# Kernel optimization log

Measured on AMD Instinct MI355X. Metric: run time of the kernel, lower is better.

## Reference

```python
import jax, jax.numpy as jnp
import numpy as np

COMMITMENT_COST = 0.25


def setup_inputs() -> dict:
    key = jax.random.key(0)
    k1, k2 = jax.random.split(key)
    B, H, W, D, K = 64, 32, 32, 64, 512
    inputs = jax.random.normal(k1, (B, H, W, D), dtype=jnp.float32)
    # VarianceScaling(): truncated normal with stddev ~ sqrt(1/fan_in); plain normal scaled is fine as init
    embeddings = jax.random.normal(k2, (D, K), dtype=jnp.float32) * np.float32(1.0 / np.sqrt(D))
    return {"inputs": inputs, "embeddings": embeddings}


def reference(inputs, embeddings):
    D = embeddings.shape[0]
    flat = inputs.reshape(-1, D)  # [N, D]
    distances = (
        jnp.sum(flat * flat, axis=1, keepdims=True)
        - 2.0 * (flat @ embeddings)
        + jnp.sum(embeddings * embeddings, axis=0, keepdims=True)
    )
    encoding_indices = jnp.argmin(distances, axis=1)  # [N]
    # one-hot @ embeddings.T is just a gather of rows of embeddings.T
    quantized = jnp.take(embeddings.T, encoding_indices, axis=0).reshape(inputs.shape)
    loss = (
        jnp.mean(jnp.square(jax.lax.stop_gradient(quantized) - inputs))
        + COMMITMENT_COST * jnp.mean(jnp.square(quantized - jax.lax.stop_gradient(inputs)))
    )
    # straight-through estimator
    quantized_st = inputs + jax.lax.stop_gradient(quantized - inputs)
    indices = encoding_indices.reshape(inputs.shape[:-1])
    return quantized_st, indices, loss
```

## Files before the change

### kernel.cpp

```cpp
#include <hip/hip_runtime.h>
#include <stdint.h>


#define DDIM 64
#define KCODES 512

typedef __bf16 bf16x8 __attribute__((ext_vector_type(8)));
typedef float f32x4 __attribute__((ext_vector_type(4)));

#define GLOAD_LDS16(gp, lp)                                        \
  __builtin_amdgcn_global_load_lds(                                \
      (const __attribute__((address_space(1))) void*)(gp),         \
      (__attribute__((address_space(3))) void*)(lp), 16, 0, 0)


__device__ __forceinline__ void split3(float f, __bf16& h1, __bf16& h2,
                                       __bf16& h3) {
  h1 = (__bf16)f;
  float r1 = f - (float)h1;
  h2 = (__bf16)r1;
  float r2 = r1 - (float)h2;
  h3 = (__bf16)r2;
}

__global__ void vq_prep_m(const float* __restrict__ w,
                          bf16x8* __restrict__ wb,
                          float* __restrict__ wT, float* __restrict__ wsq,
                          float* __restrict__ loss_out) {
  const int b = blockIdx.x, t = threadIdx.x;
  if (b < 16) {
    const int c = b * 256 + t;
    const int ctg = c >> 7;
    const int h = (c >> 6) & 1;
    const int L = c & 63, quad = L >> 4, col = L & 15;
    bf16x8 v1, v2, v3;
#pragma unroll
    for (int j = 0; j < 8; ++j) {
      float f = w[(quad * 8 + 32 * h + j) * KCODES + ctg * 16 + col];
      __bf16 h1, h2, h3; split3(f, h1, h2, h3);
      v1[j] = h1; v2[j] = h2; v3[j] = h3;
    }
    const int base = (ctg >> 2) * 24 + (ctg & 3) * 6 + h * 3;
    wb[(base + 0) * 64 + L] = v1;
    wb[(base + 1) * 64 + L] = v2;
    wb[(base + 2) * 64 + L] = v3;
  } else {
    int g = (b - 16) * 256 + t;
    int d = g >> 9, k = g & 511;
    wT[k * DDIM + d] = w[g];
    if (g < KCODES) {
      float s = 0.f;
      for (int dd = 0; dd < DDIM; ++dd) {
        float tv = w[dd * KCODES + g];
        s = fmaf(tv, tv, s);
      }
      wsq[g] = s;
    }
    if (g == 0) *loss_out = 0.f;
  }
}

__global__ __launch_bounds__(512, 4)
void vq_mfma(const float* __restrict__ x_in, const bf16x8* __restrict__ wb,
             const float* __restrict__ wsq, const float* __restrict__ wT,
             float* __restrict__ out_q, float* __restrict__ out_idx,
             float* __restrict__ loss_out) {
  __shared__ bf16x8 ldsb[3072];
  __shared__ unsigned long long sm_key[128];
  __shared__ float sm_xsq[128];
  __shared__ unsigned int sm_idx[128];
  __shared__ float sm_loss[128];

  const int t = threadIdx.x, b = blockIdx.x;
  const int wv = t >> 6, L = t & 63, quad = L >> 4, col = L & 15;

  const int sgbase = wv * 64 + L;

#pragma unroll
  for (int i = 0; i < 3; ++i)
    GLOAD_LDS16(wb + i * 512 + sgbase, &ldsb[i * 512 + wv * 64]);

  bf16x8 a[3][2];
  {
    const float* xr =
        x_in + ((size_t)b * 128 + wv * 16 + col) * DDIM + quad * 8;
    float ssq = 0.f;
#pragma unroll
    for (int h = 0; h < 2; ++h) {
      float4 p0 = *(const float4*)(xr + 32 * h);
      float4 p1 = *(const float4*)(xr + 32 * h + 4);
      float f[8] = {p0.x, p0.y, p0.z, p0.w, p1.x, p1.y, p1.z, p1.w};
      bf16x8 v1, v2, v3;
#pragma unroll
      for (int j = 0; j < 8; ++j) {
        ssq = fmaf(f[j], f[j], ssq);
        __bf16 h1, h2, h3; split3(f[j], h1, h2, h3);
        v1[j] = h1; v2[j] = h2; v3[j] = h3;
      }
      a[0][h] = v1; a[1][h] = v2; a[2][h] = v3;
    }
    ssq += __shfl_xor(ssq, 16, 64);
    ssq += __shfl_xor(ssq, 32, 64);
    if (quad == 0) sm_xsq[wv * 16 + col] = ssq;
  }

  float best[4];
  int bidx[4];
#pragma unroll
  for (int r = 0; r < 4; ++r) { best[r] = 3.0e38f; bidx[r] = 0; }

#pragma unroll 1
  for (int ph = 0; ph < 8; ++ph) {
    __syncthreads();
    float wq0 = wsq[ph * 64 + col];
    float wq1 = wsq[ph * 64 + 16 + col];
    float wq2 = wsq[ph * 64 + 32 + col];
    float wq3 = wsq[ph * 64 + 48 + col];
    if (ph < 7) {
      const bf16x8* src = wb + (ph + 1) * 1536 + sgbase;
      bf16x8* dst = &ldsb[((ph + 1) & 1) * 1536 + wv * 64];
#pragma unroll
      for (int i = 0; i < 3; ++i)
        GLOAD_LDS16(src + i * 512, dst + i * 512);
    }

    const bf16x8* bufp = ldsb + (ph & 1) * 1536;
    __builtin_amdgcn_s_setprio(1);
#pragma unroll
    for (int ct = 0; ct < 4; ++ct) {
      f32x4 acc = {0.f, 0.f, 0.f, 0.f};
#pragma unroll
      for (int h = 0; h < 2; ++h) {
        bf16x8 b0 = bufp[(ct * 6 + h * 3 + 0) * 64 + L];
        bf16x8 b1 = bufp[(ct * 6 + h * 3 + 1) * 64 + L];
        bf16x8 b2 = bufp[(ct * 6 + h * 3 + 2) * 64 + L];
        acc = __builtin_amdgcn_mfma_f32_16x16x32_bf16(a[0][h], b0, acc, 0, 0, 0);
        acc = __builtin_amdgcn_mfma_f32_16x16x32_bf16(a[0][h], b1, acc, 0, 0, 0);
        acc = __builtin_amdgcn_mfma_f32_16x16x32_bf16(a[1][h], b0, acc, 0, 0, 0);
        acc = __builtin_amdgcn_mfma_f32_16x16x32_bf16(a[1][h], b1, acc, 0, 0, 0);
        acc = __builtin_amdgcn_mfma_f32_16x16x32_bf16(a[0][h], b2, acc, 0, 0, 0);
        acc = __builtin_amdgcn_mfma_f32_16x16x32_bf16(a[2][h], b0, acc, 0, 0, 0);
      }
      int code = ph * 64 + ct * 16 + col;
      float wq = (ct == 0) ? wq0 : (ct == 1) ? wq1 : (ct == 2) ? wq2 : wq3;
#pragma unroll
      for (int r = 0; r < 4; ++r) {
        float d0 = fmaf(acc[r], -2.0f, wq);
        if (d0 < best[r]) { best[r] = d0; bidx[r] = code; }
      }
    }
    __builtin_amdgcn_s_setprio(0);
  }

#pragma unroll
  for (int r = 0; r < 4; ++r) {
    unsigned int ub = __float_as_uint(best[r]);
    ub = (ub & 0x80000000u) ? ~ub : (ub | 0x80000000u);
    unsigned long long key = ((unsigned long long)ub << 32) |
                             (unsigned long long)(unsigned int)bidx[r];
#pragma unroll
    for (int off = 1; off < 16; off <<= 1) {
      unsigned long long o = __shfl_xor(key, off, 64);
      key = o < key ? o : key;
    }
    if (col == 0)
      sm_key[wv * 16 + quad * 4 + r] = key;
  }
  __syncthreads();

  if (t < 128) {
    unsigned long long k = sm_key[t];
    unsigned int idx = (unsigned int)k;
    sm_idx[t] = idx;
    out_idx[(size_t)b * 128 + t] = (float)idx;
    unsigned int u = (unsigned int)(k >> 32);
    u = (u & 0x80000000u) ? (u & 0x7FFFFFFFu) : ~u;
    sm_loss[t] = (__uint_as_float(u) + sm_xsq[t]) * (1.25f / 4194304.0f);
  }
  __syncthreads();

  float4* dst = (float4*)(out_q + (size_t)b * 8192);
#pragma unroll
  for (int i = 0; i < 4; ++i) {
    int e4 = i * 512 + t;
    int p2 = e4 >> 4, d4 = e4 & 15;
    unsigned int idx = sm_idx[p2];
    dst[e4] = ((const float4*)(wT + (size_t)idx * DDIM))[d4];
  }

  if (t < 64) {
    float s = sm_loss[t] + sm_loss[t + 64];
#pragma unroll
    for (int off = 32; off > 0; off >>= 1) s += __shfl_down(s, off);
    if (t == 0) atomicAdd(loss_out, s);
  }
}


__global__ void vq_prep(const float* __restrict__ w, float* __restrict__ wT,
                        float* __restrict__ wsq, float* __restrict__ loss_out) {
  int g = blockIdx.x * 256 + threadIdx.x;
  int d = g >> 9, k = g & 511;
  wT[k * DDIM + d] = w[g];
  if (g < KCODES) {
    float s = 0.f;
    for (int dd = 0; dd < DDIM; ++dd) {
      float t = w[dd * KCODES + g];
      s = fmaf(t, t, s);
    }
    wsq[g] = s;
  }
  if (g == 0) *loss_out = 0.f;
}

__global__ __launch_bounds__(512, 8)
void vq_main(const float* __restrict__ x_in, const float* __restrict__ w,
             const float* __restrict__ wT, const float* __restrict__ wsq,
             float* __restrict__ out_q, float* __restrict__ out_idx,
             float* __restrict__ loss_out) {
  __shared__ float xs[DDIM][65];
  __shared__ unsigned long long sm_key[8][64];
  __shared__ unsigned int sm_idx[64];
  __shared__ float sm_sx[64];
  __shared__ float sm_loss[64];

  const int t = threadIdx.x;
  const int pb = blockIdx.x;
  const int wv = __builtin_amdgcn_readfirstlane(t >> 6);
  const int lane = t & 63;

  {
    const float4* src = (const float4*)(x_in + (size_t)pb * 4096);
#pragma unroll
    for (int i = 0; i < 2; ++i) {
      int e4 = i * 512 + t;
      float4 v = src[e4];
      int e = e4 << 2;
      int pt = e >> 6, d = e & 63;
      xs[d][pt] = v.x; xs[d + 1][pt] = v.y;
      xs[d + 2][pt] = v.z; xs[d + 3][pt] = v.w;
    }
  }
  __syncthreads();

  const int kbase = wv << 6;
  float best = 3.0e38f;
  int bidx = 0;
  float sx = 0.f;

#pragma unroll 1
  for (int kb = 0; kb < 2; ++kb) {
    const int k0 = kbase + (kb << 5);
    const float* wp = w + k0;
    float acc[32];
#pragma unroll
    for (int c = 0; c < 32; ++c) acc[c] = 0.f;
#pragma unroll 1
    for (int d8 = 0; d8 < 8; ++d8) {
      float xv[8];
#pragma unroll
      for (int dd = 0; dd < 8; ++dd) xv[dd] = xs[(d8 << 3) + dd][lane];
      if (wv == 0 && kb == 0) {
#pragma unroll
        for (int dd = 0; dd < 8; ++dd) sx = fmaf(xv[dd], xv[dd], sx);
      }
#pragma unroll
      for (int dd = 0; dd < 8; ++dd) {
        const float* wd = wp + (((d8 << 3) + dd) << 9);
#pragma unroll
        for (int c = 0; c < 32; ++c) acc[c] = fmaf(wd[c], xv[dd], acc[c]);
      }
    }
#pragma unroll
    for (int c = 0; c < 32; ++c) {
      float dist = fmaf(acc[c], -2.0f, wsq[k0 + c]);
      if (dist < best) { best = dist; bidx = k0 + c; }
    }
  }

  unsigned int ub = __float_as_uint(best);
  ub = (ub & 0x80000000u) ? ~ub : (ub | 0x80000000u);
  sm_key[wv][lane] =
      ((unsigned long long)ub << 32) | (unsigned long long)(unsigned int)bidx;
  if (wv == 0) sm_sx[lane] = sx;
  __syncthreads();

  if (t < 64) {
    unsigned long long k = sm_key[0][t];
#pragma unroll
    for (int wi = 1; wi < 8; ++wi) {
      unsigned long long k2 = sm_key[wi][t];
      k = k2 < k ? k2 : k;
    }
    unsigned int idx = (unsigned int)k;
    sm_idx[t] = idx;
    out_idx[((size_t)pb << 6) + t] = (float)idx;
    unsigned int u = (unsigned int)(k >> 32);
    u = (u & 0x80000000u) ? (u & 0x7FFFFFFFu) : ~u;
    sm_loss[t] = (__uint_as_float(u) + sm_sx[t]) * (1.25f / 4194304.0f);
  }
  __syncthreads();

  float4* dst = (float4*)(out_q + (size_t)pb * 4096);
#pragma unroll
  for (int i = 0; i < 2; ++i) {
    int e4 = i * 512 + t;
    int p2 = e4 >> 4, d4 = e4 & 15;
    unsigned int idx = sm_idx[p2];
    dst[e4] = ((const float4*)(wT + (size_t)idx * DDIM))[d4];
  }

  if (t < 64) {
    float s = sm_loss[t];
#pragma unroll
    for (int off = 32; off > 0; off >>= 1) s += __shfl_down(s, off);
    if (t == 0) atomicAdd(loss_out, s);
  }
}

extern "C" void kernel_launch(void* const* d_in, const int* in_sizes, int n_in,
                              void* d_out, int out_size, void* d_ws, size_t ws_size,
                              hipStream_t stream) {
  const float* x = (const float*)d_in[0];
  const float* w = (const float*)d_in[1];

  float* out_q = (float*)d_out;
  float* out_idx = out_q + 4194304;
  float* loss_out = out_q + 4259840;

  char* ws = (char*)d_ws;
  if (ws_size >= 329728) {
    bf16x8* wbp = (bf16x8*)(ws);
    float* wT = (float*)(ws + 196608);
    float* wsq = (float*)(ws + 327680);
    vq_prep_m<<<144, 256, 0, stream>>>(w, wbp, wT, wsq, loss_out);
    vq_mfma<<<512, 512, 0, stream>>>(x, wbp, wsq, wT, out_q, out_idx,
                                     loss_out);
  } else {
    float* wT = (float*)(ws);
    float* wsq = (float*)(ws + 131072);
    vq_prep<<<128, 256, 0, stream>>>(w, wT, wsq, loss_out);
    vq_main<<<1024, 512, 0, stream>>>(x, w, wT, wsq, out_q, out_idx,
                                      loss_out);
  }
}
```

Baseline: 97.62 us.

## Triple-buffer codebook LDS loads with explicit waitcnt and dual accumulators

Moves the codebook staging from double to triple buffering, prefetching two phases ahead and using explicit vmcnt waits with a raw barrier in place of __syncthreads. All wsq values are preloaded into registers up front and the phase loop is fully unrolled. Each MFMA chain is split into two independent accumulators, shortening dependency chains before summing them. In exchange the kernel uses more LDS and registers, which may limit occupancy under the launch bounds, and summing two accumulators slightly changes floating-point rounding.

```diff
diff --git a/kernel.cpp b/kernel.cpp
--- a/kernel.cpp
+++ b/kernel.cpp
@@ -65,7 +65,7 @@
              const float* __restrict__ wsq, const float* __restrict__ wT,
              float* __restrict__ out_q, float* __restrict__ out_idx,
              float* __restrict__ loss_out) {
-  __shared__ bf16x8 ldsb[3072];
+  __shared__ bf16x8 ldsb[4608];
   __shared__ unsigned long long sm_key[128];
   __shared__ float sm_xsq[128];
   __shared__ unsigned int sm_idx[128];
@@ -79,6 +79,9 @@
 #pragma unroll
   for (int i = 0; i < 3; ++i)
     GLOAD_LDS16(wb + i * 512 + sgbase, &ldsb[i * 512 + wv * 64]);
+#pragma unroll
+  for (int i = 0; i < 3; ++i)
+    GLOAD_LDS16(wb + 1536 + i * 512 + sgbase, &ldsb[1536 + i * 512 + wv * 64]);
 
   bf16x8 a[3][2];
   {
@@ -104,48 +107,69 @@
     if (quad == 0) sm_xsq[wv * 16 + col] = ssq;
   }
 
+  float wq[8][4];
+#pragma unroll
+  for (int p = 0; p < 8; ++p)
+#pragma unroll
+    for (int c = 0; c < 4; ++c) wq[p][c] = wsq[p * 64 + c * 16 + col];
+
   float best[4];
   int bidx[4];
 #pragma unroll
   for (int r = 0; r < 4; ++r) { best[r] = 3.0e38f; bidx[r] = 0; }
 
-#pragma unroll 1
+#pragma unroll
   for (int ph = 0; ph < 8; ++ph) {
-    __syncthreads();
-    float wq0 = wsq[ph * 64 + col];
-    float wq1 = wsq[ph * 64 + 16 + col];
-    float wq2 = wsq[ph * 64 + 32 + col];
-    float wq3 = wsq[ph * 64 + 48 + col];
-    if (ph < 7) {
-      const bf16x8* src = wb + (ph + 1) * 1536 + sgbase;
-      bf16x8* dst = &ldsb[((ph + 1) & 1) * 1536 + wv * 64];
+    if (ph < 7)
+      asm volatile("s_waitcnt vmcnt(3) lgkmcnt(0)" ::: "memory");
+    else
+      asm volatile("s_waitcnt vmcnt(0) lgkmcnt(0)" ::: "memory");
+    __builtin_amdgcn_sched_barrier(0);
+    __builtin_amdgcn_s_barrier();
+    __builtin_amdgcn_sched_barrier(0);
+
+    if (ph < 6) {
+      const bf16x8* src = wb + (ph + 2) * 1536 + sgbase;
+      bf16x8* dstl = &ldsb[((ph + 2) % 3) * 1536 + wv * 64];
 #pragma unroll
       for (int i = 0; i < 3; ++i)
-        GLOAD_LDS16(src + i * 512, dst + i * 512);
-    }
-
-    const bf16x8* bufp = ldsb + (ph & 1) * 1536;
+        GLOAD_LDS16(src + i * 512, dstl + i * 512);
+    }
+
+    const bf16x8* bufp = ldsb + (ph % 3) * 1536;
     __builtin_amdgcn_s_setprio(1);
 #pragma unroll
     for (int ct = 0; ct < 4; ++ct) {
-      f32x4 acc = {0.f, 0.f, 0.f, 0.f};
-#pragma unroll
-      for (int h = 0; h < 2; ++h) {
-        bf16x8 b0 = bufp[(ct * 6 + h * 3 + 0) * 64 + L];
-        bf16x8 b1 = bufp[(ct * 6 + h * 3 + 1) * 64 + L];
-        bf16x8 b2 = bufp[(ct * 6 + h * 3 + 2) * 64 + L];
-        acc = __builtin_amdgcn_mfma_f32_16x16x32_bf16(a[0][h], b0, acc, 0, 0, 0);
-        acc = __builtin_amdgcn_mfma_f32_16x16x32_bf16(a[0][h], b1, acc, 0, 0, 0);
-        acc = __builtin_amdgcn_mfma_f32_16x16x32_bf16(a[1][h], b0, acc, 0, 0, 0);
-        acc = __builtin_amdgcn_mfma_f32_16x16x32_bf16(a[1][h], b1, acc, 0, 0, 0);
-        acc = __builtin_amdgcn_mfma_f32_16x16x32_bf16(a[0][h], b2, acc, 0, 0, 0);
-        acc = __builtin_amdgcn_mfma_f32_16x16x32_bf16(a[2][h], b0, acc, 0, 0, 0);
-      }
+      f32x4 aA = {0.f, 0.f, 0.f, 0.f};
+      f32x4 aB = {0.f, 0.f, 0.f, 0.f};
+      {
+        bf16x8 b0 = bufp[(ct * 6 + 0) * 64 + L];
+        bf16x8 b1 = bufp[(ct * 6 + 1) * 64 + L];
+        bf16x8 b2 = bufp[(ct * 6 + 2) * 64 + L];
+        aA = __builtin_amdgcn_mfma_f32_16x16x32_bf16(a[0][0], b0, aA, 0, 0, 0);
+        aA = __builtin_amdgcn_mfma_f32_16x16x32_bf16(a[0][0], b1, aA, 0, 0, 0);
+        aA = __builtin_amdgcn_mfma_f32_16x16x32_bf16(a[1][0], b0, aA, 0, 0, 0);
+        aA = __builtin_amdgcn_mfma_f32_16x16x32_bf16(a[1][0], b1, aA, 0, 0, 0);
+        aA = __builtin_amdgcn_mfma_f32_16x16x32_bf16(a[0][0], b2, aA, 0, 0, 0);
+        aA = __builtin_amdgcn_mfma_f32_16x16x32_bf16(a[2][0], b0, aA, 0, 0, 0);
+      }
+      {
+        bf16x8 b0 = bufp[(ct * 6 + 3) * 64 + L];
+        bf16x8 b1 = bufp[(ct * 6 + 4) * 64 + L];
+        bf16x8 b2 = bufp[(ct * 6 + 5) * 64 + L];
+        aB = __builtin_amdgcn_mfma_f32_16x16x32_bf16(a[0][1], b0, aB, 0, 0, 0);
+        aB = __builtin_amdgcn_mfma_f32_16x16x32_bf16(a[0][1], b1, aB, 0, 0, 0);
+        aB = __builtin_amdgcn_mfma_f32_16x16x32_bf16(a[1][1], b0, aB, 0, 0, 0);
+        aB = __builtin_amdgcn_mfma_f32_16x16x32_bf16(a[1][1], b1, aB, 0, 0, 0);
+        aB = __builtin_amdgcn_mfma_f32_16x16x32_bf16(a[0][1], b2, aB, 0, 0, 0);
+        aB = __builtin_amdgcn_mfma_f32_16x16x32_bf16(a[2][1], b0, aB, 0, 0, 0);
+      }
+      f32x4 acc = aA + aB;
       int code = ph * 64 + ct * 16 + col;
-      float wq = (ct == 0) ? wq0 : (ct == 1) ? wq1 : (ct == 2) ? wq2 : wq3;
+      float wqv = wq[ph][ct];
 #pragma unroll
       for (int r = 0; r < 4; ++r) {
-        float d0 = fmaf(acc[r], -2.0f, wq);
+        float d0 = fmaf(acc[r], -2.0f, wqv);
         if (d0 < best[r]) { best[r] = d0; bidx[r] = code; }
       }
     }
```

After: 115.3 us. 1.18x slower.
